# Optimization experiments

Hardware: AMD Instinct MI355X
Metric: run time of the kernel (lower is better)

Reference implementation:

```python
import jax, jax.numpy as jnp
import numpy as np

LOW_THRESH = 0.3
HIGH_THRESH = 0.7
BATCH_SIZE = 256
NUM_POS = BATCH_SIZE // 2   # 128; guaranteed <= total_pos since B2=512 GT boxes are scattered positive
NUM_NEG = BATCH_SIZE - NUM_POS


def _xcycwh_to_x1y1x2y2(b):
    xc, yc, w, h = b[..., 0], b[..., 1], b[..., 2], b[..., 3]
    return jnp.stack([xc - w / 2, yc - h / 2, xc + w / 2, yc + h / 2], axis=-1)


def box_iou(box1, box2):
    # box1: (1, B1, 4), box2: (1, B2, 4) in (xc, yc, w, h) -> iou (1, B1, B2)
    area1 = box1[..., 2] * box1[..., 3]              # (1, B1)
    area2 = box2[..., 2] * box2[..., 3]              # (1, B2)
    c1 = _xcycwh_to_x1y1x2y2(box1)[:, :, None, :]    # (1, B1, 1, 4)
    c2 = _xcycwh_to_x1y1x2y2(box2)[:, None, :, :]    # (1, 1, B2, 4)
    x0 = jnp.maximum(c1[..., 0], c2[..., 0])
    y0 = jnp.maximum(c1[..., 1], c2[..., 1])
    x1 = jnp.minimum(c1[..., 2], c2[..., 2])
    y1 = jnp.minimum(c1[..., 3], c2[..., 3])
    inter = jnp.maximum(x1 - x0, 0.0) * jnp.maximum(y1 - y0, 0.0)  # (1, B1, B2)
    return inter / (area1[:, :, None] + area2[:, None, :] - inter)


def setup_inputs() -> dict:
    key = jax.random.key(0)
    k1, k2, k3, k4 = jax.random.split(key, 4)
    return {
        "input_boxes": jax.random.uniform(k1, (1, 50000, 4), dtype=jnp.float32),
        "target_boxes": jax.random.uniform(k2, (1, 512, 4), dtype=jnp.float32),
        "pos_noise": jax.random.uniform(k3, (50000,), dtype=jnp.float32),
        "neg_noise": jax.random.uniform(k4, (50000,), dtype=jnp.float32),
    }


def reference(input_boxes, target_boxes, pos_noise, neg_noise):
    ious = box_iou(input_boxes, target_boxes)        # (1, B1, B2)
    input_max_iou = jnp.max(ious, axis=2)            # (1, B1) best GT per proposal
    input_idx = jnp.argmax(ious, axis=2)             # (1, B1)
    target_idx = jnp.argmax(ious, axis=1)            # (1, B2) best proposal per GT

    pos_mask = input_max_iou[0] > HIGH_THRESH        # (B1,)
    neg_mask = input_max_iou[0] < LOW_THRESH
    # each GT's best-matching proposal is forced positive (scatter_)
    pos_mask = pos_mask.at[target_idx[0]].set(True)
    neg_mask = neg_mask.at[target_idx[0]].set(False)
    # fallback: if no negatives at all, negatives = complement of positives
    neg_mask = jnp.where(jnp.sum(neg_mask) == 0, ~pos_mask, neg_mask)

    # uniform sampling without replacement == top-k over iid uniform noise restricted to the mask
    pos_scores = jnp.where(pos_mask, pos_noise, -1.0)
    _, pos_input_idx = jax.lax.top_k(pos_scores, NUM_POS)      # (NUM_POS,)
    neg_scores = jnp.where(neg_mask, neg_noise, -1.0)
    _, neg_input_idx = jax.lax.top_k(neg_scores, NUM_NEG)      # (NUM_NEG,)

    pos_target_idx = input_idx[0][pos_input_idx]               # (NUM_POS,)
    return pos_input_idx, pos_target_idx, neg_input_idx
```

## Files before the change

kernel.cpp:

```cpp
#include <hip/hip_runtime.h>
#include <stdint.h>

#pragma clang fp contract(off)

typedef unsigned long long ull;

#define HIGHT 0.7f
#define LOWT  0.3f
#define KSEL  128
#define CAP   2048
#define MAXGT 512
#define TPB   256
#define CHUNK 32
#define TJ    64
#define SMP   72
#define NLAD  7

__device__ __constant__ float LADV[NLAD] = {0.998f, 0.99f, 0.95f, 0.8f, 0.5f, 0.25f, 0.0625f};

__device__ __forceinline__ float iou_pair(float ax0, float ay0, float ax1, float ay1, float aarea,
                                          float bx0, float by0, float bx1, float by1, float barea){
#pragma clang fp contract(off)
  float x0 = fmaxf(ax0, bx0);
  float y0 = fmaxf(ay0, by0);
  float x1 = fminf(ax1, bx1);
  float y1 = fminf(ay1, by1);
  float dx = fmaxf(x1 - x0, 0.0f);
  float dy = fmaxf(y1 - y0, 0.0f);
  float inter = dx * dy;
  float uni = (aarea + barea) - inter;
  return inter / uni;
}

__global__ __launch_bounds__(TPB)
void fused_iou(const float4* __restrict__ boxes, const float4* __restrict__ gts,
               int n1, int n2, int nblk,
               float* __restrict__ max_iou, int* __restrict__ input_idx,
               ull* __restrict__ colpart, int* __restrict__ forced,
               int* __restrict__ cnts_part, int* __restrict__ cnts,
               const float* __restrict__ pn, const float* __restrict__ nn)
{
#pragma clang fp contract(off)
  const int b = blockIdx.x, t = threadIdx.x;

  for (int x = b * TPB + t; x < n1; x += nblk * TPB) forced[x] = 0;
  if (b == 0 && t < 32) cnts[t] = 0;

  __shared__ float4 gc[MAXGT];
  __shared__ float  ga[MAXGT];
  __shared__ float  smat[CHUNK * SMP];
  __shared__ float  sm[CHUNK];

  for (int j = t; j < n2; j += TPB){
    float4 g = gts[j];
    float hw = g.z * 0.5f, hh = g.w * 0.5f;
    gc[j] = make_float4(g.x - hw, g.y - hh, g.x + hw, g.y + hh);
    ga[j] = g.z * g.w;
  }
  __syncthreads();

  const int lo = b * CHUNK;
  int cr = n1 - lo; if (cr > CHUNK) cr = CHUNK; if (cr < 0) cr = 0;

  const int pi = t >> 3, q = t & 7;
  const bool valid = (pi < cr);
  float px0 = 0, py0 = 0, px1 = 0, py1 = 0, pa = 0;
  if (valid){
    float4 pb = boxes[lo + pi];
    float hw = pb.z * 0.5f, hh = pb.w * 0.5f;
    px0 = pb.x - hw; py0 = pb.y - hh; px1 = pb.x + hw; py1 = pb.y + hh;
    pa = pb.z * pb.w;
  }
  float vA = -1.0f, vB = -1.0f; int jA = 0, jB = 0;

  for (int tb = 0; tb < n2; tb += TJ){
    const int tn = min(TJ, n2 - tb);
    if (valid){
      const int jlim = tb + tn;
      int s = 0;
      for (;; s += 2){
        int j0 = tb + q + 8 * s;
        int j1 = j0 + 8;
        if (j1 < jlim){
          float4 g0 = gc[j0]; float a0 = ga[j0];
          float4 g1 = gc[j1]; float a1 = ga[j1];
          float u = iou_pair(px0, py0, px1, py1, pa, g0.x, g0.y, g0.z, g0.w, a0);
          float w = iou_pair(px0, py0, px1, py1, pa, g1.x, g1.y, g1.z, g1.w, a1);
          smat[pi * SMP + (j0 - tb)] = u;
          smat[pi * SMP + (j1 - tb)] = w;
          if (u > vA){ vA = u; jA = j0; }
          if (w > vB){ vB = w; jB = j1; }
        } else {
          if (j0 < jlim){
            float4 g0 = gc[j0]; float a0 = ga[j0];
            float u = iou_pair(px0, py0, px1, py1, pa, g0.x, g0.y, g0.z, g0.w, a0);
            smat[pi * SMP + (j0 - tb)] = u;
            if (u > vA){ vA = u; jA = j0; }
          }
          break;
        }
      }
    }
    __syncthreads();
    {
      const int jloc = t >> 2, qp = t & 3;
      if (jloc < tn){
        float cv = -1.0f; int cp = 0;
        for (int p = qp; p < cr; p += 4){
          float v = smat[p * SMP + jloc];
          if (v > cv){ cv = v; cp = p; }
        }
        #pragma unroll
        for (int m = 1; m <= 2; m <<= 1){
          float ov = __shfl_xor(cv, m, 64);
          int   op = __shfl_xor(cp, m, 64);
          if (ov > cv || (ov == cv && op < cp)){ cv = ov; cp = op; }
        }
        if (qp == 0){
          colpart[(size_t)b * n2 + (tb + jloc)] =
            ((ull)__float_as_uint(cv) << 32) | (ull)(unsigned)~(unsigned)(lo + cp);
        }
      }
    }
    __syncthreads();
  }

  if (vB > vA || (vB == vA && jB < jA)){ vA = vB; jA = jB; }
  #pragma unroll
  for (int m = 1; m <= 4; m <<= 1){
    float ov = __shfl_xor(vA, m, 64);
    int   oj = __shfl_xor(jA, m, 64);
    if (ov > vA || (ov == vA && oj < jA)){ vA = ov; jA = oj; }
  }
  if (valid && q == 0){
    max_iou[lo + pi] = vA;
    input_idx[lo + pi] = jA;
    sm[pi] = vA;
  }
  __syncthreads();

  if (t < 64){
    const bool vld = (t < cr);
    float m = vld ? sm[t] : -1.0f;
    bool pos = vld && (m > HIGHT);
    bool nm  = vld && (m < LOWT);
    bool np  = vld && !(m > HIGHT);
    float sp = pos ? pn[lo + t] : -1.0f;
    float sn = (nm || np) ? nn[lo + t] : -1.0f;
    int c[24];
    c[0] = __popcll(__ballot(pos));
    c[1] = __popcll(__ballot(nm));
    c[2] = __popcll(__ballot(np));
    #pragma unroll
    for (int k = 0; k < NLAD; ++k){
      float L = LADV[k];
      c[3 + k]  = __popcll(__ballot(pos && sp > L));
      c[10 + k] = __popcll(__ballot(nm  && sn > L));
      c[17 + k] = __popcll(__ballot(np  && sn > L));
    }
    if (t == 0){
      #pragma unroll
      for (int k = 0; k < 24; ++k) cnts_part[b * 24 + k] = c[k];
    }
  }
}

__global__ __launch_bounds__(TPB)
void colfix_kernel(const ull* __restrict__ colpart, int n1, int n2, int nblk,
                   const float* __restrict__ max_iou,
                   const float* __restrict__ pn, const float* __restrict__ nn,
                   int* __restrict__ forced, const int* __restrict__ cnts_part,
                   int* __restrict__ cnts)
{
  const int t = threadIdx.x;
  __shared__ ull red[TPB];
  __shared__ int ired[TPB];

  if (blockIdx.x < (unsigned)n2){
    const int jj = blockIdx.x;
    ull m = 0;
    for (int x = t; x < nblk; x += TPB){
      ull v = colpart[(size_t)x * n2 + jj];
      if (v > m) m = v;
    }
    red[t] = m;
    __syncthreads();
    for (int s = TPB >> 1; s > 0; s >>= 1){
      if (t < s && red[t + s] > red[t]) red[t] = red[t + s];
      __syncthreads();
    }
    if (t == 0){
      unsigned idx = ~(unsigned)(red[0] & 0xFFFFFFFFull);
      if (idx < (unsigned)n1){
        int old = atomicExch(&forced[idx], 1);
        if (old == 0){
          float m2 = max_iou[idx];
          if (!(m2 > HIGHT)){
            float sp = pn[idx];
            float sn = nn[idx];
            atomicAdd(&cnts[0], 1);
            atomicAdd(&cnts[2], -1);
            #pragma unroll
            for (int k = 0; k < NLAD; ++k){
              float L = LADV[k];
              if (sp > L) atomicAdd(&cnts[3 + k], 1);
              if (sn > L) atomicAdd(&cnts[17 + k], -1);
            }
            if (m2 < LOWT){
              atomicAdd(&cnts[1], -1);
              #pragma unroll
              for (int k = 0; k < NLAD; ++k)
                if (sn > LADV[k]) atomicAdd(&cnts[10 + k], -1);
            }
          }
        }
      }
    }
  } else {
    const int k = blockIdx.x - n2;
    int s = 0;
    for (int x = t; x < nblk; x += TPB) s += cnts_part[x * 24 + k];
    ired[t] = s;
    __syncthreads();
    for (int st = TPB >> 1; st > 0; st >>= 1){
      if (t < st) ired[t] += ired[t + st];
      __syncthreads();
    }
    if (t == 0 && ired[0]) atomicAdd(&cnts[k], ired[0]);
  }
}

__device__ __forceinline__ float pick_tau(const int* lad, int tot){
  if (tot <= CAP) return -1.0f;
  for (int k = 0; k < NLAD; ++k)
    if (lad[k] >= KSEL) return LADV[k];
  return -1.0f;
}

__global__ __launch_bounds__(TPB)
void collect_kernel(const float* __restrict__ max_iou, const int* __restrict__ forced,
                    const float* __restrict__ pn, const float* __restrict__ nn,
                    int n1, int* __restrict__ cnts, ull* __restrict__ cand)
{
  __shared__ int s_c[24];
  const int t = threadIdx.x;
  if (t < 24) s_c[t] = cnts[t];
  __syncthreads();
  const bool fb = (s_c[1] == 0);
  const int totP = s_c[0];
  const int totN = fb ? s_c[2] : s_c[1];
  const float tauP = pick_tau(&s_c[3], totP);
  const float tauN = pick_tau(fb ? &s_c[17] : &s_c[10], totN);

  const int i = blockIdx.x * TPB + t;
  if (i >= n1) return;
  float m = max_iou[i];
  bool f = forced[i] != 0;
  bool pos = (m > HIGHT) || f;
  if (pos){
    float sc = pn[i];
    if (sc > tauP){
      int p = atomicAdd(&cnts[24], 1);
      if (p < CAP) cand[p] = ((ull)(__float_as_uint(sc) + 1u) << 32) | (ull)(unsigned)~(unsigned)i;
    }
  } else if (totP < KSEL && i < 2 * KSEL){
    int p = atomicAdd(&cnts[24], 1);
    if (p < CAP) cand[p] = (ull)(unsigned)~(unsigned)i;
  }
  bool seln = fb ? (!pos) : ((m < LOWT) && !f);
  if (seln){
    float sc = nn[i];
    if (sc > tauN){
      int p = atomicAdd(&cnts[25], 1);
      if (p < CAP) cand[CAP + p] = ((ull)(__float_as_uint(sc) + 1u) << 32) | (ull)(unsigned)~(unsigned)i;
    }
  } else if (totN < KSEL && i < 2 * KSEL){
    int p = atomicAdd(&cnts[25], 1);
    if (p < CAP) cand[CAP + p] = (ull)(unsigned)~(unsigned)i;
  }
}

__global__ __launch_bounds__(1024)
void select_kernel(const ull* __restrict__ cand, const int* __restrict__ cnts,
                   const int* __restrict__ input_idx, int* __restrict__ out)
{
  const int t = threadIdx.x;
  const bool isPos = (blockIdx.x == 0);
  __shared__ ull keys[CAP];
  int n = cnts[isPos ? 24 : 25]; if (n > CAP) n = CAP;
  for (int x = t; x < n; x += 1024)
    keys[x] = cand[(isPos ? 0 : CAP) + x];
  __syncthreads();
  ull mk[2]; int mr[2]; int ne = 0;
  for (int x = t; x < n; x += 1024){ mk[ne] = keys[x]; mr[ne] = 0; ++ne; }
  for (int o = 0; o < n; ++o){
    ull ko = keys[o];
    if (ne > 0) mr[0] += (ko > mk[0]);
    if (ne > 1) mr[1] += (ko > mk[1]);
  }
  for (int e = 0; e < ne; ++e){
    int r = mr[e];
    if (r < KSEL){
      unsigned idx = ~(unsigned)(mk[e] & 0xFFFFFFFFull);
      if (isPos){ out[r] = (int)idx; out[KSEL + r] = input_idx[idx]; }
      else        out[2 * KSEL + r] = (int)idx;
    }
  }
}

extern "C" void kernel_launch(void* const* d_in, const int* in_sizes, int n_in,
                              void* d_out, int out_size, void* d_ws, size_t ws_size,
                              hipStream_t stream){
  const float4* boxes = (const float4*)d_in[0];
  const float4* gts   = (const float4*)d_in[1];
  const float* pos_noise = (const float*)d_in[2];
  const float* neg_noise = (const float*)d_in[3];
  const int n1 = in_sizes[0] / 4;
  const int n2 = in_sizes[1] / 4;
  int* out = (int*)d_out;

  char* ws = (char*)d_ws;
  size_t off = 0;
  auto carve = [&](size_t bytes) -> char* {
    char* p = ws + off;
    off = (off + bytes + 255) & ~(size_t)255;
    return p;
  };
  const int nblk = (n1 + CHUNK - 1) / CHUNK;
  float* max_iou   = (float*)carve((size_t)n1 * 4);
  int*   input_idx = (int*)  carve((size_t)n1 * 4);
  ull*   colpart   = (ull*)  carve((size_t)nblk * n2 * 8);
  int*   forced    = (int*)  carve((size_t)n1 * 4);
  int*   cnts_part = (int*)  carve((size_t)nblk * 24 * 4);
  int*   cnts      = (int*)  carve(32 * 4);
  ull*   cand      = (ull*)  carve((size_t)2 * CAP * 8);

  const int gb = (n1 + TPB - 1) / TPB;
  fused_iou<<<nblk, TPB, 0, stream>>>(boxes, gts, n1, n2, nblk,
                                      max_iou, input_idx, colpart, forced,
                                      cnts_part, cnts, pos_noise, neg_noise);
  colfix_kernel<<<n2 + 24, TPB, 0, stream>>>(colpart, n1, n2, nblk, max_iou,
                                             pos_noise, neg_noise, forced, cnts_part, cnts);
  collect_kernel<<<gb, TPB, 0, stream>>>(max_iou, forced, pos_noise, neg_noise,
                                         n1, cnts, cand);
  select_kernel<<<2, 1024, 0, stream>>>(cand, cnts, input_idx, out);
}
```

Measured before the change: 137.1 us.

## Double-buffer IoU tile matrix so row and column passes overlap with one barrier

```diff
diff --git a/kernel.cpp b/kernel.cpp
--- a/kernel.cpp
+++ b/kernel.cpp
@@ -48,7 +48,7 @@
 
   __shared__ float4 gc[MAXGT];
   __shared__ float  ga[MAXGT];
-  __shared__ float  smat[CHUNK * SMP];
+  __shared__ float  smat[2 * CHUNK * SMP];
   __shared__ float  sm[CHUNK];
 
   for (int j = t; j < n2; j += TPB){
@@ -57,7 +57,6 @@
     gc[j] = make_float4(g.x - hw, g.y - hh, g.x + hw, g.y + hh);
     ga[j] = g.z * g.w;
   }
-  __syncthreads();
 
   const int lo = b * CHUNK;
   int cr = n1 - lo; if (cr > CHUNK) cr = CHUNK; if (cr < 0) cr = 0;
@@ -71,61 +70,70 @@
     px0 = pb.x - hw; py0 = pb.y - hh; px1 = pb.x + hw; py1 = pb.y + hh;
     pa = pb.z * pb.w;
   }
-  float vA = -1.0f, vB = -1.0f; int jA = 0, jB = 0;
-
-  for (int tb = 0; tb < n2; tb += TJ){
+  float v0 = -1.0f, v1 = -1.0f, v2 = -1.0f, v3 = -1.0f;
+  int   i0 = 0, i1 = 0, i2 = 0, i3 = 0;
+  __syncthreads();
+
+  const int ntiles = (n2 + TJ - 1) / TJ;
+
+  auto row_tile = [&](int tb, float* buf){
+    if (!valid) return;
     const int tn = min(TJ, n2 - tb);
-    if (valid){
-      const int jlim = tb + tn;
-      int s = 0;
-      for (;; s += 2){
-        int j0 = tb + q + 8 * s;
-        int j1 = j0 + 8;
-        if (j1 < jlim){
-          float4 g0 = gc[j0]; float a0 = ga[j0];
-          float4 g1 = gc[j1]; float a1 = ga[j1];
-          float u = iou_pair(px0, py0, px1, py1, pa, g0.x, g0.y, g0.z, g0.w, a0);
-          float w = iou_pair(px0, py0, px1, py1, pa, g1.x, g1.y, g1.z, g1.w, a1);
-          smat[pi * SMP + (j0 - tb)] = u;
-          smat[pi * SMP + (j1 - tb)] = w;
-          if (u > vA){ vA = u; jA = j0; }
-          if (w > vB){ vB = w; jB = j1; }
-        } else {
-          if (j0 < jlim){
-            float4 g0 = gc[j0]; float a0 = ga[j0];
-            float u = iou_pair(px0, py0, px1, py1, pa, g0.x, g0.y, g0.z, g0.w, a0);
-            smat[pi * SMP + (j0 - tb)] = u;
-            if (u > vA){ vA = u; jA = j0; }
-          }
-          break;
-        }
-      }
-    }
+    const int base = pi * SMP;
+    #pragma unroll
+    for (int r = 0; r < 2; ++r){
+      int ja = q + 8 * (4 * r + 0);
+      int jb = q + 8 * (4 * r + 1);
+      int jc = q + 8 * (4 * r + 2);
+      int jd = q + 8 * (4 * r + 3);
+      bool ea = ja < tn, eb = jb < tn, ec = jc < tn, ed = jd < tn;
+      float ua = -1.0f, ub = -1.0f, uc = -1.0f, ud = -1.0f;
+      if (ea){ float4 g = gc[tb + ja]; ua = iou_pair(px0, py0, px1, py1, pa, g.x, g.y, g.z, g.w, ga[tb + ja]); }
+      if (eb){ float4 g = gc[tb + jb]; ub = iou_pair(px0, py0, px1, py1, pa, g.x, g.y, g.z, g.w, ga[tb + jb]); }
+      if (ec){ float4 g = gc[tb + jc]; uc = iou_pair(px0, py0, px1, py1, pa, g.x, g.y, g.z, g.w, ga[tb + jc]); }
+      if (ed){ float4 g = gc[tb + jd]; ud = iou_pair(px0, py0, px1, py1, pa, g.x, g.y, g.z, g.w, ga[tb + jd]); }
+      if (ea){ buf[base + ja] = ua; if (ua > v0){ v0 = ua; i0 = tb + ja; } }
+      if (eb){ buf[base + jb] = ub; if (ub > v1){ v1 = ub; i1 = tb + jb; } }
+      if (ec){ buf[base + jc] = uc; if (uc > v2){ v2 = uc; i2 = tb + jc; } }
+      if (ed){ buf[base + jd] = ud; if (ud > v3){ v3 = ud; i3 = tb + jd; } }
+    }
+  };
+
+  auto col_tile = [&](int tb, const float* buf){
+    const int jloc = t >> 2, qp = t & 3;
+    const int tn = min(TJ, n2 - tb);
+    if (jloc >= tn) return;
+    float cv = -1.0f; int cp = 0;
+    for (int p = qp; p < cr; p += 4){
+      float v = buf[p * SMP + jloc];
+      if (v > cv){ cv = v; cp = p; }
+    }
+    #pragma unroll
+    for (int m = 1; m <= 2; m <<= 1){
+      float ov = __shfl_xor(cv, m, 64);
+      int   op = __shfl_xor(cp, m, 64);
+      if (ov > cv || (ov == cv && op < cp)){ cv = ov; cp = op; }
+    }
+    if (qp == 0){
+      colpart[(size_t)b * n2 + (tb + jloc)] =
+        ((ull)__float_as_uint(cv) << 32) | (ull)(unsigned)~(unsigned)(lo + cp);
+    }
+  };
+
+  row_tile(0, smat);
+  __syncthreads();
+  for (int k = 0; k < ntiles; ++k){
+    float* cur = smat + (k & 1) * (CHUNK * SMP);
+    float* nxt = smat + ((k + 1) & 1) * (CHUNK * SMP);
+    if (k + 1 < ntiles) row_tile((k + 1) * TJ, nxt);
+    col_tile(k * TJ, cur);
     __syncthreads();
-    {
-      const int jloc = t >> 2, qp = t & 3;
-      if (jloc < tn){
-        float cv = -1.0f; int cp = 0;
-        for (int p = qp; p < cr; p += 4){
-          float v = smat[p * SMP + jloc];
-          if (v > cv){ cv = v; cp = p; }
-        }
-        #pragma unroll
-        for (int m = 1; m <= 2; m <<= 1){
-          float ov = __shfl_xor(cv, m, 64);
-          int   op = __shfl_xor(cp, m, 64);
-          if (ov > cv || (ov == cv && op < cp)){ cv = ov; cp = op; }
-        }
-        if (qp == 0){
-          colpart[(size_t)b * n2 + (tb + jloc)] =
-            ((ull)__float_as_uint(cv) << 32) | (ull)(unsigned)~(unsigned)(lo + cp);
-        }
-      }
-    }
-    __syncthreads();
-  }
-
-  if (vB > vA || (vB == vA && jB < jA)){ vA = vB; jA = jB; }
+  }
+
+  float vA = v0; int jA = i0;
+  if (v1 > vA || (v1 == vA && i1 < jA)){ vA = v1; jA = i1; }
+  if (v2 > vA || (v2 == vA && i2 < jA)){ vA = v2; jA = i2; }
+  if (v3 > vA || (v3 == vA && i3 < jA)){ vA = v3; jA = i3; }
   #pragma unroll
   for (int m = 1; m <= 4; m <<= 1){
     float ov = __shfl_xor(vA, m, 64);
```

After: 139.0 us. About the same (+1.3%).
